# Kernel tuning notes

Measured on AMD Instinct MI355X. Metric: run time of the kernel, lower is better.

Reference implementation:

```python
import jax, jax.numpy as jnp
import numpy as np

D_MODEL = 1024
N_HEADS = 16
D_HEAD = D_MODEL // N_HEADS
D_FF = 4 * D_MODEL
B, T = 2, 2048
LN_EPS = 1e-5


def layer_norm(x, g, b):
    mu = jnp.mean(x, axis=-1, keepdims=True)
    var = jnp.mean(jnp.square(x - mu), axis=-1, keepdims=True)
    return (x - mu) * jax.lax.rsqrt(var + LN_EPS) * g + b


def setup_inputs() -> dict:
    key = jax.random.key(0)
    ks = jax.random.split(key, 8)
    s = lambda fan: 1.0 / np.sqrt(fan)
    return {
        "x": jax.random.normal(ks[0], (B, T, D_MODEL), dtype=jnp.float32),
        "ln1_g": jnp.ones((D_MODEL,), jnp.float32),
        "ln1_b": jnp.zeros((D_MODEL,), jnp.float32),
        "Wqkv": jax.random.normal(ks[1], (D_MODEL, 3 * D_MODEL), jnp.float32) * s(D_MODEL),
        "Wout": jax.random.normal(ks[2], (D_MODEL, D_MODEL), jnp.float32) * s(D_MODEL),
        "ln2_g": jnp.ones((D_MODEL,), jnp.float32),
        "ln2_b": jnp.zeros((D_MODEL,), jnp.float32),
        "W1": jax.random.normal(ks[3], (D_MODEL, D_FF), jnp.float32) * s(D_MODEL),
        "b1": jnp.zeros((D_FF,), jnp.float32),
        "W2": jax.random.normal(ks[4], (D_FF, D_MODEL), jnp.float32) * s(D_FF),
        "b2": jnp.zeros((D_MODEL,), jnp.float32),
    }


def attention(x, Wqkv, Wout):
    Bx, Tx, C = x.shape
    qkv = x @ Wqkv  # [B,T,3C]
    q, k, v = jnp.split(qkv, 3, axis=-1)
    q = q.reshape(Bx, Tx, N_HEADS, D_HEAD)
    k = k.reshape(Bx, Tx, N_HEADS, D_HEAD)
    v = v.reshape(Bx, Tx, N_HEADS, D_HEAD)
    scores = jnp.einsum('bqhd,bkhd->bhqk', q, k) / np.sqrt(D_HEAD).astype(np.float32)
    causal = jnp.tril(jnp.ones((Tx, Tx), dtype=bool))
    scores = jnp.where(causal, scores, -jnp.inf)
    attn = jax.nn.softmax(scores, axis=-1)
    out = jnp.einsum('bhqk,bkhd->bqhd', attn, v).reshape(Bx, Tx, C)
    return out @ Wout


def reference(x, ln1_g, ln1_b, Wqkv, Wout, ln2_g, ln2_b, W1, b1, W2, b2):
    x = x + attention(layer_norm(x, ln1_g, ln1_b), Wqkv, Wout)
    h = layer_norm(x, ln2_g, ln2_b)
    h = jax.nn.gelu(h @ W1 + b1, approximate=False) @ W2 + b2
    return x + h
```

## Files before the change

### kernel.cpp

```cpp
#include <hip/hip_runtime.h>
#include <math.h>

typedef __bf16 bf16;
typedef __bf16 bf16x4 __attribute__((ext_vector_type(4)));
typedef __bf16 bf16x8 __attribute__((ext_vector_type(8)));
typedef float  f32x4  __attribute__((ext_vector_type(4)));

#define MFMA16(a,b,c) __builtin_amdgcn_mfma_f32_16x16x32_bf16((a),(b),(c),0,0,0)

static __device__ __forceinline__ bf16x8 combine8(const bf16* plo, const bf16* phi) {
  bf16x4 lo = *(const bf16x4*)plo;
  bf16x4 hi = *(const bf16x4*)phi;
  return __builtin_shufflevector(lo, hi, 0, 1, 2, 3, 4, 5, 6, 7);
}

__global__ __launch_bounds__(256) void transpose_cast(const float* __restrict__ W,
                                                      bf16* __restrict__ WT,
                                                      int K, int N) {
  __shared__ float t[32][33];
  int n0 = blockIdx.x * 32, k0 = blockIdx.y * 32;
  int tx = threadIdx.x, ty = threadIdx.y;
#pragma unroll
  for (int i = 0; i < 32; i += 8)
    t[ty + i][tx] = W[(size_t)(k0 + ty + i) * N + n0 + tx];
  __syncthreads();
#pragma unroll
  for (int i = 0; i < 32; i += 8)
    WT[(size_t)(n0 + ty + i) * K + k0 + tx] = (bf16)t[tx][ty + i];
}

__global__ __launch_bounds__(256) void ln_kernel(const float* __restrict__ X,
                                                 const float* __restrict__ g,
                                                 const float* __restrict__ bta,
                                                 bf16* __restrict__ out) {
  int row  = blockIdx.x * 4 + (threadIdx.x >> 6);
  int lane = threadIdx.x & 63;
  const float4* x4 = (const float4*)(X + (size_t)row * 1024);
  float4 v[4];
  float s = 0.f, ss = 0.f;
#pragma unroll
  for (int i = 0; i < 4; ++i) {
    v[i] = x4[i * 64 + lane];
    s  += v[i].x + v[i].y + v[i].z + v[i].w;
    ss += v[i].x * v[i].x + v[i].y * v[i].y + v[i].z * v[i].z + v[i].w * v[i].w;
  }
#pragma unroll
  for (int off = 1; off < 64; off <<= 1) {
    s  += __shfl_xor(s, off, 64);
    ss += __shfl_xor(ss, off, 64);
  }
  float mu  = s * (1.0f / 1024.0f);
  float var = ss * (1.0f / 1024.0f) - mu * mu;
  float rs  = rsqrtf(var + 1e-5f);
  bf16* orow = out + (size_t)row * 1024;
#pragma unroll
  for (int i = 0; i < 4; ++i) {
    int c = i * 256 + lane * 4;
    bf16x4 pk;
    pk[0] = (bf16)((v[i].x - mu) * rs * g[c + 0] + bta[c + 0]);
    pk[1] = (bf16)((v[i].y - mu) * rs * g[c + 1] + bta[c + 1]);
    pk[2] = (bf16)((v[i].z - mu) * rs * g[c + 2] + bta[c + 2]);
    pk[3] = (bf16)((v[i].w - mu) * rs * g[c + 3] + bta[c + 3]);
    *(bf16x4*)(orow + c) = pk;
  }
}

template <int NR>
static __device__ __forceinline__ void stage2(const bf16* const* srcs, int koff,
                                              unsigned char* lds_base, int wv) {
#pragma unroll
  for (int i = 0; i < NR; ++i)
    __builtin_amdgcn_global_load_lds(
        (const __attribute__((address_space(1))) void*)(srcs[i] + koff),
        (__attribute__((address_space(3))) void*)(lds_base + (wv * (NR * 8) + i * 8) * 128),
        16, 0, 0);
}

static __device__ __forceinline__ bf16x8 frag_ld(const unsigned char* lds_base,
                                                 int r, int u) {
  return *(const bf16x8*)(lds_base + r * 128 + (((u ^ (r & 7)) & 7) << 4));
}

static __device__ __forceinline__ float gelu_tanh(float v) {
  float t = 0.7978845608028654f * (v + 0.044715f * v * v * v);
  t = fminf(t, 15.0f);
  float e = __builtin_amdgcn_exp2f(2.8853900817779268f * t);
  float th = (e - 1.0f) * __builtin_amdgcn_rcpf(e + 1.0f);
  return 0.5f * v * (1.0f + th);
}

template <int EPI, int BM>
__global__ __launch_bounds__(256) void gemm_bt(const bf16* __restrict__ A,
                                               const bf16* __restrict__ BT,
                                               int K, int N, int gx,
                                               const float* __restrict__ bias,
                                               const float* __restrict__ res,
                                               bf16* __restrict__ outb,
                                               float* __restrict__ outf) {
  constexpr int MI = BM / 32;
  constexpr int ANR = BM / 32;
  constexpr int TILE = (BM + 128) * 128;
  __shared__ unsigned char smem[TILE * 2];
  int nwg = gridDim.x, bid = blockIdx.x;
  int nb = (bid & 7) * (nwg >> 3) + (bid >> 3);
  int bx = nb % gx, by = nb / gx;
  int brow = by * BM, bcol = bx * 128;
  int tid = threadIdx.x, wv = tid >> 6, lane = tid & 63;
  int l15 = lane & 15, l4 = lane >> 4;
  int wm = wv >> 1, wn = wv & 1;
  f32x4 acc[MI][4] = {};

  int sr = lane >> 3;
  int su = (lane & 7) ^ sr;
  const bf16* aptr[ANR];
#pragma unroll
  for (int i = 0; i < ANR; ++i)
    aptr[i] = A + (size_t)(brow + wv * (ANR * 8) + i * 8 + sr) * K + su * 8;
  const bf16* bptr[4];
#pragma unroll
  for (int i = 0; i < 4; ++i)
    bptr[i] = BT + (size_t)(bcol + wv * 32 + i * 8 + sr) * K + su * 8;

  stage2<ANR>(aptr, 0, smem, wv);
  stage2<4>(bptr, 0, smem + BM * 128, wv);
  __syncthreads();
  int cur = 0;
  for (int k0 = 0; k0 < K; k0 += 64) {
    unsigned char* sc = smem + cur * TILE;
    if (k0 + 64 < K) {
      unsigned char* sn = smem + (cur ^ 1) * TILE;
      stage2<ANR>(aptr, k0 + 64, sn, wv);
      stage2<4>(bptr, k0 + 64, sn + BM * 128, wv);
    }
    unsigned char* As = sc;
    unsigned char* Bs = sc + BM * 128;
#pragma unroll
    for (int ks = 0; ks < 2; ++ks) {
      bf16x8 af[MI], bfr[4];
#pragma unroll
      for (int mi = 0; mi < MI; ++mi)
        af[mi] = frag_ld(As, wm * (BM / 2) + mi * 16 + l15, ks * 4 + l4);
#pragma unroll
      for (int ni = 0; ni < 4; ++ni)
        bfr[ni] = frag_ld(Bs, wn * 64 + ni * 16 + l15, ks * 4 + l4);
#pragma unroll
      for (int mi = 0; mi < MI; ++mi)
#pragma unroll
        for (int ni = 0; ni < 4; ++ni)
          acc[mi][ni] = MFMA16(af[mi], bfr[ni], acc[mi][ni]);
    }
    __syncthreads();
    cur ^= 1;
  }
#pragma unroll
  for (int mi = 0; mi < MI; ++mi) {
#pragma unroll
    for (int ni = 0; ni < 4; ++ni) {
      int col  = bcol + wn * 64 + ni * 16 + l15;
      int row0 = brow + wm * (BM / 2) + mi * 16 + l4 * 4;
#pragma unroll
      for (int r = 0; r < 4; ++r) {
        int row = row0 + r;
        float v = acc[mi][ni][r];
        if (EPI == 1) {
          v += bias[col];
          v = gelu_tanh(v);
        }
        if (EPI == 2) v += res[(size_t)row * N + col];
        if (EPI == 3) v += bias[col] + res[(size_t)row * N + col];
        if (EPI == 0 || EPI == 1) outb[(size_t)row * N + col] = (bf16)v;
        else                      outf[(size_t)row * N + col] = v;
      }
    }
  }
}

__global__ __launch_bounds__(256) void pack_kv(const bf16* __restrict__ qkv,
                                               bf16* __restrict__ kpack,
                                               bf16* __restrict__ vpack) {
  int blk = blockIdx.x;
  int wv = threadIdx.x >> 6, lane = threadIdx.x & 63;
  int l15 = lane & 15, l4 = lane >> 4;
  int ch = (blk & 15) * 4 + wv;
  int bh = blk >> 4;
  int b = bh >> 4, h = bh & 15;
  const bf16* kq = qkv + (size_t)b * 2048 * 3072 + 1024 + h * 64;
  const bf16* vq = kq + 1024;
#pragma unroll
  for (int fr = 0; fr < 4; ++fr) {
    int key = ch * 32 + ((fr >> 1) << 4) + l15;
    int dbase = ((fr & 1) << 5) + l4 * 4;
    bf16x8 v = combine8(kq + (size_t)key * 3072 + dbase,
                        kq + (size_t)key * 3072 + dbase + 16);
    *(bf16x8*)(kpack + ((size_t)(bh * 64 + ch) * 4 + fr) * 512 + lane * 8) = v;
  }
#pragma unroll
  for (int db = 0; db < 4; ++db) {
    int d = db * 16 + l15;
    bf16x8 v;
#pragma unroll
    for (int j = 0; j < 8; ++j) {
      int key = ch * 32 + l4 * 4 + (j & 3) + ((j >> 2) << 4);
      v[j] = vq[(size_t)key * 3072 + d];
    }
    *(bf16x8*)(vpack + ((size_t)(bh * 64 + ch) * 4 + db) * 512 + lane * 8) = v;
  }
}

static __device__ __forceinline__ void proc_chunk(
    const bf16x8* __restrict__ kf, const bf16x8* __restrict__ vf,
    const bf16x8 (* __restrict__ qf)[2], f32x4 (* __restrict__ o)[4],
    float* __restrict__ lsum, bool diag, int l15, int l4) {
  const float SC = 0.125f * 1.4426950408889634f;
#pragma unroll
  for (int f = 0; f < 2; ++f) {
    f32x4 c0 = {0.f, 0.f, 0.f, 0.f}, c1 = {0.f, 0.f, 0.f, 0.f};
    c0 = MFMA16(kf[0], qf[f][0], c0);
    c0 = MFMA16(kf[1], qf[f][1], c0);
    c1 = MFMA16(kf[2], qf[f][0], c1);
    c1 = MFMA16(kf[3], qf[f][1], c1);
    bf16x8 pf;
    float ls = 0.f;
#pragma unroll
    for (int r = 0; r < 4; ++r) {
      float e0 = __builtin_amdgcn_exp2f(c0[r] * SC);
      float e1 = __builtin_amdgcn_exp2f(c1[r] * SC);
      if (diag) {
        int qg = f * 16 + l15;
        int key = l4 * 4 + r;
        if (key > qg)      e0 = 0.f;
        if (key + 16 > qg) e1 = 0.f;
      }
      ls += e0 + e1;
      pf[r]     = (bf16)e0;
      pf[4 + r] = (bf16)e1;
    }
    lsum[f] += ls;
    o[f][0] = MFMA16(vf[0], pf, o[f][0]);
    o[f][1] = MFMA16(vf[1], pf, o[f][1]);
    o[f][2] = MFMA16(vf[2], pf, o[f][2]);
    o[f][3] = MFMA16(vf[3], pf, o[f][3]);
  }
}

__global__ __launch_bounds__(256) void attn_kernel(const bf16* __restrict__ qkv,
                                                   const bf16* __restrict__ kpack,
                                                   const bf16* __restrict__ vpack,
                                                   bf16* __restrict__ attn_out) {
  __shared__ f32x4 obuf[48 * 64];
  __shared__ float lbuf[12 * 64];
  int bid = blockIdx.x;
  int nb = (bid & 7) * 128 + (bid >> 3);
  int bh = nb >> 5, j = nb & 31;
  int b = bh >> 4, h = bh & 15;
  int wv = threadIdx.x >> 6, lane = threadIdx.x & 63;
  int l15 = lane & 15, l4 = lane >> 4;
  int qc[2] = {j, 63 - j};
  const bf16* base = qkv + (size_t)b * 2048 * 3072;
  int d0 = l4 * 4;
  bf16x8 qf[2][2][2];
#pragma unroll
  for (int c = 0; c < 2; ++c)
#pragma unroll
    for (int f = 0; f < 2; ++f) {
      const bf16* qp = base + (size_t)(qc[c] * 32 + f * 16 + l15) * 3072 + h * 64;
      qf[c][f][0] = combine8(qp + d0,      qp + d0 + 16);
      qf[c][f][1] = combine8(qp + d0 + 32, qp + d0 + 48);
    }
  const bf16* kp0 = kpack + (size_t)bh * 64 * 2048 + lane * 8;
  const bf16* vp0 = vpack + (size_t)bh * 64 * 2048 + lane * 8;

  f32x4 o[2][2][4] = {};
  float lsum[2][2] = {};

  for (int ch = wv; ch <= qc[1]; ch += 4) {
    const bf16* kp = kp0 + (size_t)ch * 2048;
    const bf16* vp = vp0 + (size_t)ch * 2048;
    bf16x8 kf[4], vf[4];
    kf[0] = *(const bf16x8*)(kp);
    kf[1] = *(const bf16x8*)(kp + 512);
    kf[2] = *(const bf16x8*)(kp + 1024);
    kf[3] = *(const bf16x8*)(kp + 1536);
    vf[0] = *(const bf16x8*)(vp);
    vf[1] = *(const bf16x8*)(vp + 512);
    vf[2] = *(const bf16x8*)(vp + 1024);
    vf[3] = *(const bf16x8*)(vp + 1536);
    if (ch <= qc[0])
      proc_chunk(kf, vf, qf[0], o[0], lsum[0], ch == qc[0], l15, l4);
    proc_chunk(kf, vf, qf[1], o[1], lsum[1], ch == qc[1], l15, l4);
  }

#pragma unroll
  for (int s = 0; s < 4; ++s) {
    if (s == wv) continue;
    int sp = s - (s > wv ? 1 : 0);
    int c = s >> 1, f = s & 1;
#pragma unroll
    for (int db = 0; db < 4; ++db)
      obuf[((wv * 3 + sp) * 4 + db) * 64 + lane] = o[c][f][db];
    lbuf[(wv * 3 + sp) * 64 + lane] = lsum[c][f];
  }
  __syncthreads();
  {
    int c = wv >> 1, f = wv & 1;
    f32x4 osum[4];
#pragma unroll
    for (int db = 0; db < 4; ++db) osum[db] = o[c][f][db];
    float l = lsum[c][f];
#pragma unroll
    for (int ww = 0; ww < 4; ++ww) {
      if (ww == wv) continue;
      int sp = wv - (wv > ww ? 1 : 0);
#pragma unroll
      for (int db = 0; db < 4; ++db)
        osum[db] += obuf[((ww * 3 + sp) * 4 + db) * 64 + lane];
      l += lbuf[(ww * 3 + sp) * 64 + lane];
    }
    l += __shfl_xor(l, 16, 64);
    l += __shfl_xor(l, 32, 64);
    float inv = 1.0f / l;
    bf16* orow = attn_out +
                 (size_t)(b * 2048 + qc[c] * 32 + f * 16 + l15) * 1024 +
                 h * 64 + l4 * 4;
#pragma unroll
    for (int db = 0; db < 4; ++db) {
      bf16x4 pk;
      pk[0] = (bf16)(osum[db][0] * inv);
      pk[1] = (bf16)(osum[db][1] * inv);
      pk[2] = (bf16)(osum[db][2] * inv);
      pk[3] = (bf16)(osum[db][3] * inv);
      *(bf16x4*)(orow + db * 16) = pk;
    }
  }
}

extern "C" void kernel_launch(void* const* d_in, const int* in_sizes, int n_in,
                              void* d_out, int out_size, void* d_ws, size_t ws_size,
                              hipStream_t stream) {
  const float* x     = (const float*)d_in[0];
  const float* ln1g  = (const float*)d_in[1];
  const float* ln1b  = (const float*)d_in[2];
  const float* Wqkv  = (const float*)d_in[3];
  const float* Wout  = (const float*)d_in[4];
  const float* ln2g  = (const float*)d_in[5];
  const float* ln2b  = (const float*)d_in[6];
  const float* W1    = (const float*)d_in[7];
  const float* b1    = (const float*)d_in[8];
  const float* W2    = (const float*)d_in[9];
  const float* b2    = (const float*)d_in[10];
  float* out = (float*)d_out;

  char* p = (char*)d_ws;
  bf16* WqkvT = (bf16*)p; p += (size_t)3072 * 1024 * 2;
  bf16* WoutT = (bf16*)p; p += (size_t)1024 * 1024 * 2;
  bf16* W1T   = (bf16*)p; p += (size_t)4096 * 1024 * 2;
  bf16* W2T   = (bf16*)p; p += (size_t)1024 * 4096 * 2;
  bf16* hbuf  = (bf16*)p; p += (size_t)4096 * 1024 * 2;
  bf16* aobuf = (bf16*)p; p += (size_t)4096 * 1024 * 2;
  bf16* big   = (bf16*)p; p += (size_t)4096 * 4096 * 2;

  bf16* kpack = big + (size_t)4096 * 3072;
  bf16* vpack = hbuf;

  dim3 tb(32, 8);
  transpose_cast<<<dim3(96, 32),  tb, 0, stream>>>(Wqkv, WqkvT, 1024, 3072);
  transpose_cast<<<dim3(32, 32),  tb, 0, stream>>>(Wout, WoutT, 1024, 1024);
  transpose_cast<<<dim3(128, 32), tb, 0, stream>>>(W1,   W1T,   1024, 4096);
  transpose_cast<<<dim3(32, 128), tb, 0, stream>>>(W2,   W2T,   4096, 1024);

  ln_kernel<<<1024, 256, 0, stream>>>(x, ln1g, ln1b, hbuf);
  gemm_bt<0, 128><<<768, 256, 0, stream>>>(hbuf, WqkvT, 1024, 3072, 24,
                                           nullptr, nullptr, big, nullptr);
  pack_kv<<<512, 256, 0, stream>>>(big, kpack, vpack);
  attn_kernel<<<1024, 256, 0, stream>>>(big, kpack, vpack, aobuf);
  gemm_bt<2, 64><<<512, 256, 0, stream>>>(aobuf, WoutT, 1024, 1024, 8,
                                          nullptr, x, nullptr, out);
  ln_kernel<<<1024, 256, 0, stream>>>(out, ln2g, ln2b, hbuf);
  gemm_bt<1, 128><<<1024, 256, 0, stream>>>(hbuf, W1T, 1024, 4096, 32,
                                            b1, nullptr, big, nullptr);
  gemm_bt<3, 64><<<512, 256, 0, stream>>>(big, W2T, 4096, 1024, 8,
                                          b2, out, nullptr, out);
}
```

Baseline: 221.8 us.

## Merge weight transpose launches and single-buffer GEMM shared memory

Folds the four weight transpose-cast launches into one kernel that picks its matrix by block index, which removes launch overhead and the tail gaps between the small launches. The GEMM also drops its shared-memory double buffer and now loads each K tile synchronously before computing it. That halves LDS use, which may allow more resident workgroups, but global loads no longer overlap with the MFMA work.

```diff
diff --git a/kernel.cpp b/kernel.cpp
--- a/kernel.cpp
+++ b/kernel.cpp
@@ -14,11 +14,19 @@
   return __builtin_shufflevector(lo, hi, 0, 1, 2, 3, 4, 5, 6, 7);
 }
 
-__global__ __launch_bounds__(256) void transpose_cast(const float* __restrict__ W,
-                                                      bf16* __restrict__ WT,
-                                                      int K, int N) {
+__global__ __launch_bounds__(256) void transpose_all(
+    const float* __restrict__ Wqkv, bf16* __restrict__ WqkvT,
+    const float* __restrict__ Wout, bf16* __restrict__ WoutT,
+    const float* __restrict__ W1,   bf16* __restrict__ W1T,
+    const float* __restrict__ W2,   bf16* __restrict__ W2T) {
   __shared__ float t[32][33];
-  int n0 = blockIdx.x * 32, k0 = blockIdx.y * 32;
+  int b = blockIdx.x;
+  const float* W; bf16* WT; int K, N, bx, by;
+  if (b < 3072)      { W = Wqkv; WT = WqkvT; K = 1024; N = 3072;            bx = b % 96;  by = b / 96; }
+  else if (b < 4096) { W = Wout; WT = WoutT; K = 1024; N = 1024; b -= 3072; bx = b % 32;  by = b / 32; }
+  else if (b < 8192) { W = W1;   WT = W1T;   K = 1024; N = 4096; b -= 4096; bx = b % 128; by = b / 128; }
+  else               { W = W2;   WT = W2T;   K = 4096; N = 1024; b -= 8192; bx = b % 32;  by = b / 32; }
+  int n0 = bx * 32, k0 = by * 32;
   int tx = threadIdx.x, ty = threadIdx.y;
 #pragma unroll
   for (int i = 0; i < 32; i += 8)
@@ -99,8 +107,7 @@
                                                float* __restrict__ outf) {
   constexpr int MI = BM / 32;
   constexpr int ANR = BM / 32;
-  constexpr int TILE = (BM + 128) * 128;
-  __shared__ unsigned char smem[TILE * 2];
+  __shared__ unsigned char smem[(BM + 128) * 128];
   int nwg = gridDim.x, bid = blockIdx.x;
   int nb = (bid & 7) * (nwg >> 3) + (bid >> 3);
   int bx = nb % gx, by = nb / gx;
@@ -121,19 +128,12 @@
   for (int i = 0; i < 4; ++i)
     bptr[i] = BT + (size_t)(bcol + wv * 32 + i * 8 + sr) * K + su * 8;
 
-  stage2<ANR>(aptr, 0, smem, wv);
-  stage2<4>(bptr, 0, smem + BM * 128, wv);
-  __syncthreads();
-  int cur = 0;
+  unsigned char* As = smem;
+  unsigned char* Bs = smem + BM * 128;
   for (int k0 = 0; k0 < K; k0 += 64) {
-    unsigned char* sc = smem + cur * TILE;
-    if (k0 + 64 < K) {
-      unsigned char* sn = smem + (cur ^ 1) * TILE;
-      stage2<ANR>(aptr, k0 + 64, sn, wv);
-      stage2<4>(bptr, k0 + 64, sn + BM * 128, wv);
-    }
-    unsigned char* As = sc;
-    unsigned char* Bs = sc + BM * 128;
+    stage2<ANR>(aptr, k0, As, wv);
+    stage2<4>(bptr, k0, Bs, wv);
+    __syncthreads();
 #pragma unroll
     for (int ks = 0; ks < 2; ++ks) {
       bf16x8 af[MI], bfr[4];
@@ -150,7 +150,6 @@
           acc[mi][ni] = MFMA16(af[mi], bfr[ni], acc[mi][ni]);
     }
     __syncthreads();
-    cur ^= 1;
   }
 #pragma unroll
   for (int mi = 0; mi < MI; ++mi) {
@@ -362,11 +361,8 @@
   bf16* kpack = big + (size_t)4096 * 3072;
   bf16* vpack = hbuf;
 
-  dim3 tb(32, 8);
-  transpose_cast<<<dim3(96, 32),  tb, 0, stream>>>(Wqkv, WqkvT, 1024, 3072);
-  transpose_cast<<<dim3(32, 32),  tb, 0, stream>>>(Wout, WoutT, 1024, 1024);
-  transpose_cast<<<dim3(128, 32), tb, 0, stream>>>(W1,   W1T,   1024, 4096);
-  transpose_cast<<<dim3(32, 128), tb, 0, stream>>>(W2,   W2T,   4096, 1024);
+  transpose_all<<<12288, dim3(32, 8), 0, stream>>>(Wqkv, WqkvT, Wout, WoutT,
+                                                   W1, W1T, W2, W2T);
 
   ln_kernel<<<1024, 256, 0, stream>>>(x, ln1g, ln1b, hbuf);
   gemm_bt<0, 128><<<768, 256, 0, stream>>>(hbuf, WqkvT, 1024, 3072, 24,
```

Measured after the change: 235.0 us. 1.06x slower.
